# Optimization experiments

Hardware: AMD Instinct MI355X
Metric: run time of the kernel (lower is better)

The kernel has to match this reference:

```python
import jax, jax.numpy as jnp
import numpy as np

B, N, D = 4, 4096, 64

def setup_inputs() -> dict:
    key = jax.random.key(0)
    inputs = jax.random.normal(key, (B, N, D), dtype=jnp.float32)
    return {"inputs": inputs}

def reference(inputs) -> jnp.ndarray:
    # similarity = X X^T : [B, N, N]
    similarity = jnp.einsum('bnd,bmd->bnm', inputs, inputs)
    # row softmax over last axis -> adjacency
    adjacency = jax.nn.softmax(similarity, axis=-1)
    return adjacency
```

## Files before the change

kernel.cpp:

```cpp
#include <hip/hip_runtime.h>

#define B_ 4
#define N_ 4096
#define D_ 64

typedef __bf16 bf16_t;
typedef bf16_t bf16x8 __attribute__((ext_vector_type(8)));
typedef float f32x16 __attribute__((ext_vector_type(16)));

#if __has_builtin(__builtin_amdgcn_exp2f)
#define EXP2F __builtin_amdgcn_exp2f
#else
#define EXP2F exp2f
#endif

#define SQRT_LOG2E 1.2011224087864498f

__global__ void conv_pack_kernel(const float* __restrict__ X,
                                 bf16_t* __restrict__ Xp,
                                 float* __restrict__ norms) {
    const int g    = blockIdx.x * 4 + (threadIdx.x >> 6);
    const int lane = threadIdx.x & 63;
    const int mcol = lane & 31;
    const int half = lane >> 5;
    const int row  = g * 32 + mcol;

    const float* xr = X + (size_t)row * D_ + half * 8;
    float sq = 0.0f;
    #pragma unroll
    for (int i = 0; i < 4; ++i) {
        float4 u0 = *(const float4*)(xr + i * 16);
        float4 u1 = *(const float4*)(xr + i * 16 + 4);
        float v[8] = {u0.x, u0.y, u0.z, u0.w, u1.x, u1.y, u1.z, u1.w};
        bf16x8 f;
        #pragma unroll
        for (int j = 0; j < 8; ++j) {
            float x = v[j] * SQRT_LOG2E;
            sq += x * x;
            f[j] = (bf16_t)x;
        }
        *(bf16x8*)(Xp + ((size_t)(g * 4 + i) * 64 + lane) * 8) = f;
    }
    sq += __shfl_xor(sq, 32);
    if (half == 0) norms[row] = sq;
}

__global__ __launch_bounds__(512, 4) void softmax_xxt_kernel(
        const bf16_t* __restrict__ Xp,
        const float* __restrict__ norms,
        float* __restrict__ Out) {
    const int tid  = threadIdx.x;
    const int wave = tid >> 6;
    const int lane = tid & 63;
    const int b    = blockIdx.x >> 7;
    const int ga   = blockIdx.x & 127;
    const int rowbase = ga * 32;

    const bf16_t* Pb = Xp + (size_t)b * N_ * D_;
    const int mcol = lane & 31;
    const int half = lane >> 5;

    const bf16_t* ap = Pb + (size_t)ga * 2048 + (size_t)lane * 8;
    const bf16x8 a0 = *(const bf16x8*)(ap);
    const bf16x8 a1 = *(const bf16x8*)(ap + 512);
    const bf16x8 a2 = *(const bf16x8*)(ap + 1024);
    const bf16x8 a3 = *(const bf16x8*)(ap + 1536);

    float lse[16];
    {
        const float* nb = norms + b * N_ + rowbase;
        #pragma unroll
        for (int r = 0; r < 16; ++r) {
            int row = (r & 3) + 8 * (r >> 2) + 4 * half;
            lse[r] = nb[row];
        }
    }

    __shared__ float partials[8][32];

    float sums[16];
    #pragma unroll
    for (int r = 0; r < 16; ++r) sums[r] = 0.0f;

    {
        const bf16_t* bp0 = Pb + (size_t)wave * 2048 + (size_t)lane * 8;
        bf16x8 nb0 = *(const bf16x8*)(bp0);
        bf16x8 nb1 = *(const bf16x8*)(bp0 + 512);
        bf16x8 nb2 = *(const bf16x8*)(bp0 + 1024);
        bf16x8 nb3 = *(const bf16x8*)(bp0 + 1536);
        for (int t = 0; t < N_ / 256; ++t) {
            bf16x8 b0 = nb0, b1 = nb1, b2 = nb2, b3 = nb3;
            if (t + 1 < N_ / 256) {
                const bf16_t* np = Pb + (size_t)((t + 1) * 8 + wave) * 2048
                                      + (size_t)lane * 8;
                nb0 = *(const bf16x8*)(np);
                nb1 = *(const bf16x8*)(np + 512);
                nb2 = *(const bf16x8*)(np + 1024);
                nb3 = *(const bf16x8*)(np + 1536);
            }
            f32x16 acc;
            #pragma unroll
            for (int i = 0; i < 16; ++i) acc[i] = 0.0f;
            acc = __builtin_amdgcn_mfma_f32_32x32x16_bf16(a0, b0, acc, 0, 0, 0);
            acc = __builtin_amdgcn_mfma_f32_32x32x16_bf16(a1, b1, acc, 0, 0, 0);
            acc = __builtin_amdgcn_mfma_f32_32x32x16_bf16(a2, b2, acc, 0, 0, 0);
            acc = __builtin_amdgcn_mfma_f32_32x32x16_bf16(a3, b3, acc, 0, 0, 0);
            #pragma unroll
            for (int r = 0; r < 16; ++r) sums[r] += EXP2F(acc[r] - lse[r]);
        }
    }

    #pragma unroll
    for (int r = 0; r < 16; ++r) {
        float s = sums[r];
        s += __shfl_xor(s, 1);
        s += __shfl_xor(s, 2);
        s += __shfl_xor(s, 4);
        s += __shfl_xor(s, 8);
        s += __shfl_xor(s, 16);
        sums[r] = s;
    }

    if (mcol == 0) {
        #pragma unroll
        for (int r = 0; r < 16; ++r) {
            int row = (r & 3) + 8 * (r >> 2) + 4 * half;
            partials[wave][row] = sums[r];
        }
    }
    __syncthreads();

    #pragma unroll
    for (int r = 0; r < 16; ++r) {
        int row = (r & 3) + 8 * (r >> 2) + 4 * half;
        float tot = partials[0][row] + partials[1][row] +
                    partials[2][row] + partials[3][row] +
                    partials[4][row] + partials[5][row] +
                    partials[6][row] + partials[7][row];
        lse[r] += __log2f(tot);
    }

    float* outb = Out + (size_t)b * N_ * N_;
    {
        const bf16_t* bp0 = Pb + (size_t)wave * 2048 + (size_t)lane * 8;
        bf16x8 nb0 = *(const bf16x8*)(bp0);
        bf16x8 nb1 = *(const bf16x8*)(bp0 + 512);
        bf16x8 nb2 = *(const bf16x8*)(bp0 + 1024);
        bf16x8 nb3 = *(const bf16x8*)(bp0 + 1536);
        for (int t = 0; t < N_ / 256; ++t) {
            const int c0 = (t * 8 + wave) * 32;
            bf16x8 b0 = nb0, b1 = nb1, b2 = nb2, b3 = nb3;
            if (t + 1 < N_ / 256) {
                const bf16_t* np = Pb + (size_t)((t + 1) * 8 + wave) * 2048
                                      + (size_t)lane * 8;
                nb0 = *(const bf16x8*)(np);
                nb1 = *(const bf16x8*)(np + 512);
                nb2 = *(const bf16x8*)(np + 1024);
                nb3 = *(const bf16x8*)(np + 1536);
            }
            f32x16 acc;
            #pragma unroll
            for (int i = 0; i < 16; ++i) acc[i] = 0.0f;
            acc = __builtin_amdgcn_mfma_f32_32x32x16_bf16(a0, b0, acc, 0, 0, 0);
            acc = __builtin_amdgcn_mfma_f32_32x32x16_bf16(a1, b1, acc, 0, 0, 0);
            acc = __builtin_amdgcn_mfma_f32_32x32x16_bf16(a2, b2, acc, 0, 0, 0);
            acc = __builtin_amdgcn_mfma_f32_32x32x16_bf16(a3, b3, acc, 0, 0, 0);
            #pragma unroll
            for (int r = 0; r < 16; ++r) {
                int row = rowbase + (r & 3) + 8 * (r >> 2) + 4 * half;
                outb[(size_t)row * N_ + (c0 + mcol)] = EXP2F(acc[r] - lse[r]);
            }
        }
    }
}

extern "C" void kernel_launch(void* const* d_in, const int* in_sizes, int n_in,
                              void* d_out, int out_size, void* d_ws, size_t ws_size,
                              hipStream_t stream) {
    const float* X = (const float*)d_in[0];
    float* Out     = (float*)d_out;

    bf16_t* Xp    = (bf16_t*)d_ws;
    float*  norms = (float*)((char*)d_ws + (size_t)B_ * N_ * D_ * sizeof(bf16_t));

    conv_pack_kernel<<<(B_ * N_) / 128, 256, 0, stream>>>(X, Xp, norms);
    softmax_xxt_kernel<<<(B_ * N_) / 32, 512, 0, stream>>>(Xp, norms, Out);
}
```

Before: 278.0 us.

## Process two 32-row groups per block to reuse B fragments

Each block now handles 64 rows (two 32-row MFMA tiles) instead of 32, reusing each loaded B fragment for two MFMA chains in both the sum pass and the write pass. This halves key-operand loads per output and the number of blocks, and the partials buffer grows to 64 rows. The trade-off is more registers per thread (launch bounds lowered to 2 blocks per CU) and only 256 blocks, which may reduce latency hiding for the large output stores.

```diff
diff --git a/kernel.cpp b/kernel.cpp
--- a/kernel.cpp
+++ b/kernel.cpp
@@ -45,42 +45,48 @@
     if (half == 0) norms[row] = sq;
 }
 
-__global__ __launch_bounds__(512, 4) void softmax_xxt_kernel(
+__global__ __launch_bounds__(512, 2) void softmax_xxt_kernel(
         const bf16_t* __restrict__ Xp,
         const float* __restrict__ norms,
         float* __restrict__ Out) {
     const int tid  = threadIdx.x;
     const int wave = tid >> 6;
     const int lane = tid & 63;
-    const int b    = blockIdx.x >> 7;
-    const int ga   = blockIdx.x & 127;
-    const int rowbase = ga * 32;
+    const int b    = blockIdx.x >> 6;
+    const int gb   = blockIdx.x & 63;
+    const int rowbase = gb * 64;
 
     const bf16_t* Pb = Xp + (size_t)b * N_ * D_;
     const int mcol = lane & 31;
     const int half = lane >> 5;
 
-    const bf16_t* ap = Pb + (size_t)ga * 2048 + (size_t)lane * 8;
-    const bf16x8 a0 = *(const bf16x8*)(ap);
-    const bf16x8 a1 = *(const bf16x8*)(ap + 512);
-    const bf16x8 a2 = *(const bf16x8*)(ap + 1024);
-    const bf16x8 a3 = *(const bf16x8*)(ap + 1536);
-
-    float lse[16];
+    const bf16_t* ap = Pb + (size_t)(gb * 2) * 2048 + (size_t)lane * 8;
+    bf16x8 a[2][4];
+    #pragma unroll
+    for (int gi = 0; gi < 2; ++gi)
+        #pragma unroll
+        for (int k = 0; k < 4; ++k)
+            a[gi][k] = *(const bf16x8*)(ap + (size_t)gi * 2048 + k * 512);
+
+    float lse[2][16];
     {
         const float* nb = norms + b * N_ + rowbase;
         #pragma unroll
-        for (int r = 0; r < 16; ++r) {
-            int row = (r & 3) + 8 * (r >> 2) + 4 * half;
-            lse[r] = nb[row];
-        }
-    }
-
-    __shared__ float partials[8][32];
-
-    float sums[16];
-    #pragma unroll
-    for (int r = 0; r < 16; ++r) sums[r] = 0.0f;
+        for (int gi = 0; gi < 2; ++gi)
+            #pragma unroll
+            for (int r = 0; r < 16; ++r) {
+                int rl = (r & 3) + 8 * (r >> 2) + 4 * half;
+                lse[gi][r] = nb[gi * 32 + rl];
+            }
+    }
+
+    __shared__ float partials[8][64];
+
+    float sums[2][16];
+    #pragma unroll
+    for (int gi = 0; gi < 2; ++gi)
+        #pragma unroll
+        for (int r = 0; r < 16; ++r) sums[gi][r] = 0.0f;
 
     {
         const bf16_t* bp0 = Pb + (size_t)wave * 2048 + (size_t)lane * 8;
@@ -98,47 +104,57 @@
                 nb2 = *(const bf16x8*)(np + 1024);
                 nb3 = *(const bf16x8*)(np + 1536);
             }
-            f32x16 acc;
-            #pragma unroll
-            for (int i = 0; i < 16; ++i) acc[i] = 0.0f;
-            acc = __builtin_amdgcn_mfma_f32_32x32x16_bf16(a0, b0, acc, 0, 0, 0);
-            acc = __builtin_amdgcn_mfma_f32_32x32x16_bf16(a1, b1, acc, 0, 0, 0);
-            acc = __builtin_amdgcn_mfma_f32_32x32x16_bf16(a2, b2, acc, 0, 0, 0);
-            acc = __builtin_amdgcn_mfma_f32_32x32x16_bf16(a3, b3, acc, 0, 0, 0);
-            #pragma unroll
-            for (int r = 0; r < 16; ++r) sums[r] += EXP2F(acc[r] - lse[r]);
-        }
-    }
-
-    #pragma unroll
-    for (int r = 0; r < 16; ++r) {
-        float s = sums[r];
-        s += __shfl_xor(s, 1);
-        s += __shfl_xor(s, 2);
-        s += __shfl_xor(s, 4);
-        s += __shfl_xor(s, 8);
-        s += __shfl_xor(s, 16);
-        sums[r] = s;
-    }
+            #pragma unroll
+            for (int gi = 0; gi < 2; ++gi) {
+                f32x16 acc;
+                #pragma unroll
+                for (int i = 0; i < 16; ++i) acc[i] = 0.0f;
+                acc = __builtin_amdgcn_mfma_f32_32x32x16_bf16(a[gi][0], b0, acc, 0, 0, 0);
+                acc = __builtin_amdgcn_mfma_f32_32x32x16_bf16(a[gi][1], b1, acc, 0, 0, 0);
+                acc = __builtin_amdgcn_mfma_f32_32x32x16_bf16(a[gi][2], b2, acc, 0, 0, 0);
+                acc = __builtin_amdgcn_mfma_f32_32x32x16_bf16(a[gi][3], b3, acc, 0, 0, 0);
+                #pragma unroll
+                for (int r = 0; r < 16; ++r)
+                    sums[gi][r] += EXP2F(acc[r] - lse[gi][r]);
+            }
+        }
+    }
+
+    #pragma unroll
+    for (int gi = 0; gi < 2; ++gi)
+        #pragma unroll
+        for (int r = 0; r < 16; ++r) {
+            float s = sums[gi][r];
+            s += __shfl_xor(s, 1);
+            s += __shfl_xor(s, 2);
+            s += __shfl_xor(s, 4);
+            s += __shfl_xor(s, 8);
+            s += __shfl_xor(s, 16);
+            sums[gi][r] = s;
+        }
 
     if (mcol == 0) {
         #pragma unroll
+        for (int gi = 0; gi < 2; ++gi)
+            #pragma unroll
+            for (int r = 0; r < 16; ++r) {
+                int rl = (r & 3) + 8 * (r >> 2) + 4 * half;
+                partials[wave][gi * 32 + rl] = sums[gi][r];
+            }
+    }
+    __syncthreads();
+
+    #pragma unroll
+    for (int gi = 0; gi < 2; ++gi)
+        #pragma unroll
         for (int r = 0; r < 16; ++r) {
-            int row = (r & 3) + 8 * (r >> 2) + 4 * half;
-            partials[wave][row] = sums[r];
-        }
-    }
-    __syncthreads();
-
-    #pragma unroll
-    for (int r = 0; r < 16; ++r) {
-        int row = (r & 3) + 8 * (r >> 2) + 4 * half;
-        float tot = partials[0][row] + partials[1][row] +
-                    partials[2][row] + partials[3][row] +
-                    partials[4][row] + partials[5][row] +
-                    partials[6][row] + partials[7][row];
-        lse[r] += __log2f(tot);
-    }
+            int rl = gi * 32 + (r & 3) + 8 * (r >> 2) + 4 * half;
+            float tot = partials[0][rl] + partials[1][rl] +
+                        partials[2][rl] + partials[3][rl] +
+                        partials[4][rl] + partials[5][rl] +
+                        partials[6][rl] + partials[7][rl];
+            lse[gi][r] += __log2f(tot);
+        }
 
     float* outb = Out + (size_t)b * N_ * N_;
     {
@@ -158,17 +174,22 @@
                 nb2 = *(const bf16x8*)(np + 1024);
                 nb3 = *(const bf16x8*)(np + 1536);
             }
-            f32x16 acc;
-            #pragma unroll
-            for (int i = 0; i < 16; ++i) acc[i] = 0.0f;
-            acc = __builtin_amdgcn_mfma_f32_32x32x16_bf16(a0, b0, acc, 0, 0, 0);
-            acc = __builtin_amdgcn_mfma_f32_32x32x16_bf16(a1, b1, acc, 0, 0, 0);
-            acc = __builtin_amdgcn_mfma_f32_32x32x16_bf16(a2, b2, acc, 0, 0, 0);
-            acc = __builtin_amdgcn_mfma_f32_32x32x16_bf16(a3, b3, acc, 0, 0, 0);
-            #pragma unroll
-            for (int r = 0; r < 16; ++r) {
-                int row = rowbase + (r & 3) + 8 * (r >> 2) + 4 * half;
-                outb[(size_t)row * N_ + (c0 + mcol)] = EXP2F(acc[r] - lse[r]);
+            #pragma unroll
+            for (int gi = 0; gi < 2; ++gi) {
+                f32x16 acc;
+                #pragma unroll
+                for (int i = 0; i < 16; ++i) acc[i] = 0.0f;
+                acc = __builtin_amdgcn_mfma_f32_32x32x16_bf16(a[gi][0], b0, acc, 0, 0, 0);
+                acc = __builtin_amdgcn_mfma_f32_32x32x16_bf16(a[gi][1], b1, acc, 0, 0, 0);
+                acc = __builtin_amdgcn_mfma_f32_32x32x16_bf16(a[gi][2], b2, acc, 0, 0, 0);
+                acc = __builtin_amdgcn_mfma_f32_32x32x16_bf16(a[gi][3], b3, acc, 0, 0, 0);
+                #pragma unroll
+                for (int r = 0; r < 16; ++r) {
+                    int row = rowbase + gi * 32 +
+                              (r & 3) + 8 * (r >> 2) + 4 * half;
+                    outb[(size_t)row * N_ + (c0 + mcol)] =
+                        EXP2F(acc[r] - lse[gi][r]);
+                }
             }
         }
     }
@@ -184,5 +205,5 @@
     float*  norms = (float*)((char*)d_ws + (size_t)B_ * N_ * D_ * sizeof(bf16_t));
 
     conv_pack_kernel<<<(B_ * N_) / 128, 256, 0, stream>>>(X, Xp, norms);
-    softmax_xxt_kernel<<<(B_ * N_) / 32, 512, 0, stream>>>(Xp, norms, Out);
+    softmax_xxt_kernel<<<(B_ * N_) / 64, 512, 0, stream>>>(Xp, norms, Out);
 }
```

Result: no change. 278.8 us (+0.3%).
